# Kernel tuning notes

Measured on AMD Instinct MI355X. Metric: run time of the kernel, lower is better.

The kernel has to match this reference:

```python
import jax, jax.numpy as jnp
import numpy as np


def _gru(x, h0, Wi, Wh, bi, bh):
    """PyTorch-equations GRU. x: (T,B,D), Wi: (3H,D), Wh: (3H,H). Returns (ys, hT)."""
    xW = jnp.einsum('tbd,gd->tbg', x, Wi) + bi  # (T,B,3H) precomputed input proj
    def step(h, xw):
        hw = h @ Wh.T + bh
        xr, xz, xn = jnp.split(xw, 3, axis=-1)
        hr, hz, hn = jnp.split(hw, 3, axis=-1)
        r = jax.nn.sigmoid(xr + hr)
        z = jax.nn.sigmoid(xz + hz)
        n = jnp.tanh(xn + r * hn)
        h_new = (1.0 - z) * n + z * h
        return h_new, h_new
    hT, ys = jax.lax.scan(step, h0, xW)
    return ys, hT


def _bigru(x, WiF, WhF, biF, bhF, WiB, WhB, biB, bhB):
    B = x.shape[1]
    H = WhF.shape[1]
    h0 = jnp.zeros((B, H), x.dtype)
    yf, hf = _gru(x, h0, WiF, WhF, biF, bhF)
    yb, hb = _gru(x[::-1], h0, WiB, WhB, biB, bhB)
    return jnp.concatenate([yf, yb[::-1]], axis=-1), jnp.stack([hf, hb], axis=0)


def _ln(x, g, b, eps=1e-5):
    mu = x.mean(-1, keepdims=True)
    var = ((x - mu) ** 2).mean(-1, keepdims=True)
    return (x - mu) * jax.lax.rsqrt(var + eps) * g + b


def _forward(tokens, emb,
             s_WiF, s_WhF, s_biF, s_bhF, s_lnF_g, s_lnF_b,
             s_Wi_f, s_Wh_f, s_bi_f, s_bh_f, s_Wi_b, s_Wh_b, s_bi_b, s_bh_b,
             s_ln_g, s_ln_b, s_linW, s_linb,
             d_WiF, d_WhF, d_biF, d_bhF, d_lnF_g, d_lnF_b,
             d_Wi_f, d_Wh_f, d_bi_f, d_bh_f, d_Wi_b, d_Wh_b, d_bi_b, d_bh_b,
             d_ln_g, d_ln_b, out_W, out_b):
    S, T, B = tokens.shape
    H = s_WhF.shape[1]
    # sentence loop is batch-independent -> fold sentences into batch
    x = emb[tokens]                                  # (S,T,B,E)
    x = x.transpose(1, 0, 2, 3).reshape(T, S * B, -1)  # (T, S*B, E)
    h0 = jnp.zeros((S * B, H), x.dtype)
    y, _ = _gru(x, h0, s_WiF, s_WhF, s_biF, s_bhF)
    y = _ln(y, s_lnF_g, s_lnF_b)
    y, _ = _bigru(y, s_Wi_f, s_Wh_f, s_bi_f, s_bh_f, s_Wi_b, s_Wh_b, s_bi_b, s_bh_b)
    y = _ln(y, s_ln_g, s_ln_b)
    y = jnp.tanh(y @ s_linW.T + s_linb)              # (T, S*B, H)
    store = y.mean(axis=0).reshape(S, B, H)          # per-sentence mean-pooled cell
    # document-level encoder over sentence sequence
    h0d = jnp.zeros((B, H), x.dtype)
    y, _ = _gru(store, h0d, d_WiF, d_WhF, d_biF, d_bhF)
    y = _ln(y, d_lnF_g, d_lnF_b)
    y, _ = _bigru(y, d_Wi_f, d_Wh_f, d_bi_f, d_bh_f, d_Wi_b, d_Wh_b, d_bi_b, d_bh_b)
    y = _ln(y, d_ln_g, d_ln_b)
    return jax.nn.sigmoid(y @ out_W.T + out_b)       # (S, B, O)


def setup_inputs() -> dict:
    V, E, H, O = 32000, 256, 256, 2
    S, T, B = 96, 32, 32
    keys = iter(jax.random.split(jax.random.key(0), 64))
    def g(shape, scale=0.06):
        return jax.random.normal(next(keys), shape, jnp.float32) * scale
    inp = {}
    inp['tokens'] = jax.random.randint(next(keys), (S, T, B), 0, V)
    inp['emb'] = g((V, E), 0.1)
    # sentence encoder: uni GRU (E->H), LN(H), bi GRU (H->H), LN(2H), linear 2H->H
    inp['s_WiF'] = g((3 * H, E)); inp['s_WhF'] = g((3 * H, H))
    inp['s_biF'] = jnp.zeros((3 * H,)); inp['s_bhF'] = jnp.zeros((3 * H,))
    inp['s_lnF_g'] = jnp.ones((H,)); inp['s_lnF_b'] = jnp.zeros((H,))
    inp['s_Wi_f'] = g((3 * H, H)); inp['s_Wh_f'] = g((3 * H, H))
    inp['s_bi_f'] = jnp.zeros((3 * H,)); inp['s_bh_f'] = jnp.zeros((3 * H,))
    inp['s_Wi_b'] = g((3 * H, H)); inp['s_Wh_b'] = g((3 * H, H))
    inp['s_bi_b'] = jnp.zeros((3 * H,)); inp['s_bh_b'] = jnp.zeros((3 * H,))
    inp['s_ln_g'] = jnp.ones((2 * H,)); inp['s_ln_b'] = jnp.zeros((2 * H,))
    inp['s_linW'] = g((H, 2 * H)); inp['s_linb'] = jnp.zeros((H,))
    # document encoder: uni GRU (H->H), LN(H), bi GRU (H->H), LN(2H)
    inp['d_WiF'] = g((3 * H, H)); inp['d_WhF'] = g((3 * H, H))
    inp['d_biF'] = jnp.zeros((3 * H,)); inp['d_bhF'] = jnp.zeros((3 * H,))
    inp['d_lnF_g'] = jnp.ones((H,)); inp['d_lnF_b'] = jnp.zeros((H,))
    inp['d_Wi_f'] = g((3 * H, H)); inp['d_Wh_f'] = g((3 * H, H))
    inp['d_bi_f'] = jnp.zeros((3 * H,)); inp['d_bh_f'] = jnp.zeros((3 * H,))
    inp['d_Wi_b'] = g((3 * H, H)); inp['d_Wh_b'] = g((3 * H, H))
    inp['d_bi_b'] = jnp.zeros((3 * H,)); inp['d_bh_b'] = jnp.zeros((3 * H,))
    inp['d_ln_g'] = jnp.ones((2 * H,)); inp['d_ln_b'] = jnp.zeros((2 * H,))
    inp['out_W'] = g((O, 2 * H)); inp['out_b'] = jnp.zeros((O,))
    return inp


def reference(tokens, emb,
              s_WiF, s_WhF, s_biF, s_bhF, s_lnF_g, s_lnF_b,
              s_Wi_f, s_Wh_f, s_bi_f, s_bh_f, s_Wi_b, s_Wh_b, s_bi_b, s_bh_b,
              s_ln_g, s_ln_b, s_linW, s_linb,
              d_WiF, d_WhF, d_biF, d_bhF, d_lnF_g, d_lnF_b,
              d_Wi_f, d_Wh_f, d_bi_f, d_bh_f, d_Wi_b, d_Wh_b, d_bi_b, d_bh_b,
              d_ln_g, d_ln_b, out_W, out_b):
    return _forward(tokens, emb,
                    s_WiF, s_WhF, s_biF, s_bhF, s_lnF_g, s_lnF_b,
                    s_Wi_f, s_Wh_f, s_bi_f, s_bh_f, s_Wi_b, s_Wh_b, s_bi_b, s_bh_b,
                    s_ln_g, s_ln_b, s_linW, s_linb,
                    d_WiF, d_WhF, d_biF, d_bhF, d_lnF_g, d_lnF_b,
                    d_Wi_f, d_Wh_f, d_bi_f, d_bh_f, d_Wi_b, d_Wh_b, d_bi_b, d_bh_b,
                    d_ln_g, d_ln_b, out_W, out_b)
```

## Files before the change

### kernel.cpp

```cpp
#include <hip/hip_runtime.h>


typedef __bf16 bf16;
typedef __bf16 bf16x8 __attribute__((ext_vector_type(8)));
typedef __bf16 bf16x4 __attribute__((ext_vector_type(4)));
typedef float  f32x4  __attribute__((ext_vector_type(4)));

static __device__ __forceinline__ f32x4 mfma16(bf16x8 a, bf16x8 b, f32x4 c) {
  return __builtin_amdgcn_mfma_f32_16x16x32_bf16(a, b, c, 0, 0, 0);
}
static __device__ __forceinline__ float sigm(float x) { return 1.f / (1.f + __expf(-x)); }

__global__ __launch_bounds__(256) void cvt_bf16(
    const float* __restrict__ s, bf16* __restrict__ d, int n4)
{
  int i = blockIdx.x * 256 + threadIdx.x;
  if (i < n4) {
    float4 v = ((const float4*)s)[i];
    bf16x4 o;
    o[0] = (bf16)v.x; o[1] = (bf16)v.y; o[2] = (bf16)v.z; o[3] = (bf16)v.w;
    ((bf16x4*)d)[i] = o;
  }
}

__global__ __launch_bounds__(256) void conv13(
    const float* s0, const float* s1, const float* s2, const float* s3,
    const float* s4, const float* s5, const float* s6, const float* s7,
    const float* s8, const float* s9, const float* s10, const float* s11,
    const float* s12, bf16* __restrict__ dst)
{
  const float* srcs[13] = {s0,s1,s2,s3,s4,s5,s6,s7,s8,s9,s10,s11,s12};
  int m = blockIdx.y;
  int n4 = (m == 12) ? 32768 : 49152;
  int i = blockIdx.x * 256 + threadIdx.x;
  if (i >= n4) return;
  float4 v = ((const float4*)srcs[m])[i];
  bf16x4 o;
  o[0] = (bf16)v.x; o[1] = (bf16)v.y; o[2] = (bf16)v.z; o[3] = (bf16)v.w;
  ((bf16x4*)(dst + (size_t)m * 196608))[i] = o;
}

__global__ __launch_bounds__(256, 2) void gru_step(
    const bf16* __restrict__ xF, const bf16* __restrict__ hpF, bf16* __restrict__ hoF,
    const bf16* __restrict__ WiF, const bf16* __restrict__ WhF,
    const float* __restrict__ biF, const float* __restrict__ bhF,
    const bf16* __restrict__ xB, const bf16* __restrict__ hpB, bf16* __restrict__ hoB,
    const bf16* __restrict__ WiB, const bf16* __restrict__ WhB,
    const float* __restrict__ biB, const float* __restrict__ bhB,
    const int* __restrict__ tok, const bf16* __restrict__ embb, int t, int hstride)
{
  const bf16 *x, *hp, *Wi, *Wh;
  const float *bi, *bh;
  bf16* ho;
  if (blockIdx.y == 0) { x = xF; hp = hpF; ho = hoF; Wi = WiF; Wh = WhF; bi = biF; bh = bhF; }
  else                 { x = xB; hp = hpB; ho = hoB; Wi = WiB; Wh = WhB; bi = biB; bh = bhB; }

  int wv   = (threadIdx.x >> 6) + (blockIdx.x << 2);
  int cj   = (wv & 15) << 4;
  int m0   = (wv >> 4) << 5;
  int lane = threadIdx.x & 63;
  int r16  = lane & 15, g4 = lane >> 4;

  const bf16 *xp0, *xp1;
  if (x) {
    xp0 = x + (size_t)(m0 + r16) * 256;
    xp1 = xp0 + (size_t)16 * 256;
  } else {
    int n0 = m0 + r16, n1 = n0 + 16;
    int tk0 = tok[((n0 >> 5) << 10) + (t << 5) + (n0 & 31)];
    int tk1 = tok[((n1 >> 5) << 10) + (t << 5) + (n1 & 31)];
    xp0 = embb + (size_t)tk0 * 256;
    xp1 = embb + (size_t)tk1 * 256;
  }
  const bf16* wi = Wi + (size_t)(cj + r16) * 256;
  const bf16* wh = Wh + (size_t)(cj + r16) * 256;

  f32x4 Ar0 = {0,0,0,0}, Ar1 = {0,0,0,0};
  f32x4 Az0 = {0,0,0,0}, Az1 = {0,0,0,0};
  f32x4 Xn0 = {0,0,0,0}, Xn1 = {0,0,0,0};
  f32x4 Hn0 = {0,0,0,0}, Hn1 = {0,0,0,0};

#pragma unroll
  for (int kk = 0; kk < 8; kk++) {
    int k0 = kk * 32 + g4 * 8;
    bf16x8 a0 = *(const bf16x8*)(xp0 + k0);
    bf16x8 a1 = *(const bf16x8*)(xp1 + k0);
    bf16x8 wr = *(const bf16x8*)(wi + k0);
    bf16x8 wz = *(const bf16x8*)(wi + 65536 + k0);
    bf16x8 wn = *(const bf16x8*)(wi + 131072 + k0);
    Ar0 = mfma16(a0, wr, Ar0); Ar1 = mfma16(a1, wr, Ar1);
    Az0 = mfma16(a0, wz, Az0); Az1 = mfma16(a1, wz, Az1);
    Xn0 = mfma16(a0, wn, Xn0); Xn1 = mfma16(a1, wn, Xn1);
  }
  if (hp) {
    const bf16* hq0 = hp + (size_t)(m0 + r16) * hstride;
    const bf16* hq1 = hq0 + (size_t)16 * hstride;
#pragma unroll
    for (int kk = 0; kk < 8; kk++) {
      int k0 = kk * 32 + g4 * 8;
      bf16x8 a0 = *(const bf16x8*)(hq0 + k0);
      bf16x8 a1 = *(const bf16x8*)(hq1 + k0);
      bf16x8 wr = *(const bf16x8*)(wh + k0);
      bf16x8 wz = *(const bf16x8*)(wh + 65536 + k0);
      bf16x8 wn = *(const bf16x8*)(wh + 131072 + k0);
      Ar0 = mfma16(a0, wr, Ar0); Ar1 = mfma16(a1, wr, Ar1);
      Az0 = mfma16(a0, wz, Az0); Az1 = mfma16(a1, wz, Az1);
      Hn0 = mfma16(a0, wn, Hn0); Hn1 = mfma16(a1, wn, Hn1);
    }
  }

  float br = bi[cj + r16] + bh[cj + r16];
  float bz = bi[256 + cj + r16] + bh[256 + cj + r16];
  float bin = bi[512 + cj + r16], bhn = bh[512 + cj + r16];

#pragma unroll
  for (int rt = 0; rt < 2; rt++) {
    f32x4 Ar = rt ? Ar1 : Ar0, Az = rt ? Az1 : Az0;
    f32x4 Xn = rt ? Xn1 : Xn0, Hn = rt ? Hn1 : Hn0;
#pragma unroll
    for (int j = 0; j < 4; j++) {
      int orow = m0 + rt * 16 + g4 * 4 + j;
      float r = sigm(Ar[j] + br);
      float z = sigm(Az[j] + bz);
      float n = tanhf(Xn[j] + bin + r * (Hn[j] + bhn));
      float hpv = hp ? (float)hp[(size_t)orow * hstride + cj + r16] : 0.f;
      ho[(size_t)orow * hstride + cj + r16] = (bf16)((1.f - z) * n + z * hpv);
    }
  }
}

__global__ __launch_bounds__(256) void ln_rows(
    bf16* __restrict__ data, const float* __restrict__ gam, const float* __restrict__ bet,
    int rows, int D)
{
  int wid = threadIdx.x >> 6, lane = threadIdx.x & 63;
  int row = (blockIdx.x << 2) + wid;
  if (row >= rows) return;
  bf16* p = data + (size_t)row * D;
  int c = D >> 6;
  float v[8];
  float s = 0.f;
  if (c == 8) {
    bf16x8 t8 = *(const bf16x8*)(p + lane * 8);
#pragma unroll
    for (int j = 0; j < 8; j++) { v[j] = (float)t8[j]; s += v[j]; }
  } else {
    bf16x4 t4 = *(const bf16x4*)(p + lane * 4);
#pragma unroll
    for (int j = 0; j < 4; j++) { v[j] = (float)t4[j]; s += v[j]; }
#pragma unroll
    for (int j = 4; j < 8; j++) v[j] = 0.f;
  }
  float sq = 0.f;
  for (int j = 0; j < c; j++) sq += v[j] * v[j];
  for (int m = 32; m; m >>= 1) { s += __shfl_xor(s, m); sq += __shfl_xor(sq, m); }
  float invD = 1.f / (float)D;
  float mu  = s * invD;
  float var = sq * invD - mu * mu;
  float inv = rsqrtf(fmaxf(var, 0.f) + 1e-5f);
  int base = lane * c;
  for (int j = 0; j < c; j++) {
    float o = (v[j] - mu) * inv * gam[base + j] + bet[base + j];
    p[base + j] = (bf16)o;
  }
}

__global__ __launch_bounds__(256) void sent_tail(
    const bf16* __restrict__ hf, const bf16* __restrict__ hb,
    const float* __restrict__ gam, const float* __restrict__ bet,
    const bf16* __restrict__ W, const float* __restrict__ bias,
    bf16* __restrict__ store, int c, int row_base)
{
  int wave = threadIdx.x >> 6;
  int lane = threadIdx.x & 63;
  int r16 = lane & 15, g4 = lane >> 4;
  int r0 = (int)blockIdx.x << 4;
  size_t rowoff = (size_t)(r0 + r16) * 256;

  f32x4 ms0 = {0,0,0,0}, ms1 = {0,0,0,0}, ms2 = {0,0,0,0}, ms3 = {0,0,0,0};

  for (int t = 0; t < 32; t++) {
    const bf16* pf = hf + (size_t)t * c * 256 + rowoff;
    const bf16* pb = hb + (size_t)t * c * 256 + rowoff;
    bf16x8 xv[16];
    float s = 0.f, sq = 0.f;
#pragma unroll
    for (int kk = 0; kk < 16; kk++) {
      int k0 = kk * 32 + g4 * 8;
      xv[kk] = (kk < 8) ? *(const bf16x8*)(pf + k0) : *(const bf16x8*)(pb + k0 - 256);
#pragma unroll
      for (int j = 0; j < 8; j++) { float f = (float)xv[kk][j]; s += f; sq += f * f; }
    }
    s  += __shfl_xor(s, 16);  s  += __shfl_xor(s, 32);
    sq += __shfl_xor(sq, 16); sq += __shfl_xor(sq, 32);
    float mu  = s * (1.f / 512.f);
    float var = sq * (1.f / 512.f) - mu * mu;
    float inv = rsqrtf(fmaxf(var, 0.f) + 1e-5f);
#pragma unroll
    for (int kk = 0; kk < 16; kk++) {
      int k0 = kk * 32 + g4 * 8;
      float ga[8], be[8];
      *(float4*)(ga)     = *(const float4*)(gam + k0);
      *(float4*)(ga + 4) = *(const float4*)(gam + k0 + 4);
      *(float4*)(be)     = *(const float4*)(bet + k0);
      *(float4*)(be + 4) = *(const float4*)(bet + k0 + 4);
#pragma unroll
      for (int j = 0; j < 8; j++)
        xv[kk][j] = (bf16)(((float)xv[kk][j] - mu) * inv * ga[j] + be[j]);
    }
#pragma unroll
    for (int tc = 0; tc < 4; tc++) {
      int cj = wave * 64 + tc * 16;
      const bf16* wp = W + (size_t)(cj + r16) * 512;
      f32x4 acc = {0,0,0,0};
#pragma unroll
      for (int kk = 0; kk < 16; kk++)
        acc = mfma16(xv[kk], *(const bf16x8*)(wp + kk * 32 + g4 * 8), acc);
      float bb = bias[cj + r16];
      f32x4* msp = (tc == 0) ? &ms0 : (tc == 1) ? &ms1 : (tc == 2) ? &ms2 : &ms3;
#pragma unroll
      for (int j = 0; j < 4; j++) (*msp)[j] += tanhf(acc[j] + bb);
    }
  }
#pragma unroll
  for (int tc = 0; tc < 4; tc++) {
    int cj = wave * 64 + tc * 16;
    f32x4 ms = (tc == 0) ? ms0 : (tc == 1) ? ms1 : (tc == 2) ? ms2 : ms3;
#pragma unroll
    for (int j = 0; j < 4; j++) {
      int row = row_base + r0 + g4 * 4 + j;
      store[(size_t)row * 256 + cj + r16] = (bf16)(ms[j] * 0.03125f);
    }
  }
}

__global__ __launch_bounds__(256) void xw_gemm(
    const bf16* __restrict__ X,
    const bf16* __restrict__ W0, const float* __restrict__ b0, bf16* __restrict__ o0,
    const bf16* __restrict__ W1, const float* __restrict__ b1, bf16* __restrict__ o1)
{
  const bf16* W = blockIdx.y ? W1 : W0;
  const float* bias = blockIdx.y ? b1 : b0;
  bf16* out = blockIdx.y ? o1 : o0;
  int wave = (int)blockIdx.x * 4 + (threadIdx.x >> 6);
  int rt = wave / 48, ct = wave - rt * 48;
  int lane = threadIdx.x & 63;
  int r16 = lane & 15, g4 = lane >> 4;
  const bf16* ap = X + (size_t)(rt * 16 + r16) * 256;
  const bf16* wp = W + (size_t)(ct * 16 + r16) * 256;
  f32x4 acc = {0,0,0,0};
#pragma unroll
  for (int kk = 0; kk < 8; kk++) {
    int k0 = kk * 32 + g4 * 8;
    acc = mfma16(*(const bf16x8*)(ap + k0), *(const bf16x8*)(wp + k0), acc);
  }
  float bv = bias[ct * 16 + r16];
#pragma unroll
  for (int j = 0; j < 4; j++)
    out[(size_t)(rt * 16 + g4 * 4 + j) * 768 + ct * 16 + r16] = (bf16)(acc[j] + bv);
}

__global__ __launch_bounds__(1024, 4) void doc_gru(
    const bf16* __restrict__ xwF, const bf16* __restrict__ WhF_, const float* __restrict__ bhF_,
    const bf16* __restrict__ xwB, const bf16* __restrict__ WhB_, const float* __restrict__ bhB_,
    bf16* __restrict__ yout, int ostride,
    const float* __restrict__ lng, const float* __restrict__ lnb, int S)
{
  int dir = blockIdx.x;
  const bf16*  xw = dir ? xwB : xwF;
  const bf16*  Wh = dir ? WhB_ : WhF_;
  const float* bh = dir ? bhB_ : bhF_;
  int obase = dir ? 256 : 0;

  __shared__ bf16 hbuf[32][264];
  for (int idx = threadIdx.x; idx < 32 * 264; idx += 1024) ((bf16*)hbuf)[idx] = (bf16)0.f;
  __syncthreads();

  int w = threadIdx.x >> 6, lane = threadIdx.x & 63;
  int r16 = lane & 15, g4 = lane >> 4;
  int c = w * 16 + r16;
  const bf16* whp = Wh + (size_t)c * 256;
  float bhr = bh[c], bhz = bh[c + 256], bhn = bh[c + 512];

  for (int i = 0; i < S; i++) {
    int st = dir ? (S - 1 - i) : i;
    const bf16* xp = xw + (size_t)st * 24576;
    float xr[2][3][4];
#pragma unroll
    for (int rt = 0; rt < 2; rt++)
#pragma unroll
      for (int j = 0; j < 4; j++) {
        const bf16* q = xp + (size_t)(rt * 16 + g4 * 4 + j) * 768 + c;
        xr[rt][0][j] = (float)q[0];
        xr[rt][1][j] = (float)q[256];
        xr[rt][2][j] = (float)q[512];
      }
    float hp0[4], hp1[4];
#pragma unroll
    for (int j = 0; j < 4; j++) {
      hp0[j] = (float)hbuf[g4 * 4 + j][c];
      hp1[j] = (float)hbuf[16 + g4 * 4 + j][c];
    }
    f32x4 A00 = {0,0,0,0}, A01 = {0,0,0,0}, A02 = {0,0,0,0};
    f32x4 A10 = {0,0,0,0}, A11 = {0,0,0,0}, A12 = {0,0,0,0};
#pragma unroll
    for (int kk = 0; kk < 8; kk++) {
      int k0 = kk * 32 + g4 * 8;
      bf16x8 a0 = *(const bf16x8*)&hbuf[r16][k0];
      bf16x8 a1 = *(const bf16x8*)&hbuf[16 + r16][k0];
      bf16x8 w0 = *(const bf16x8*)(whp + k0);
      bf16x8 w1 = *(const bf16x8*)(whp + 65536 + k0);
      bf16x8 w2 = *(const bf16x8*)(whp + 131072 + k0);
      A00 = mfma16(a0, w0, A00); A10 = mfma16(a1, w0, A10);
      A01 = mfma16(a0, w1, A01); A11 = mfma16(a1, w1, A11);
      A02 = mfma16(a0, w2, A02); A12 = mfma16(a1, w2, A12);
    }
    float hnew[2][4];
#pragma unroll
    for (int rt = 0; rt < 2; rt++) {
      f32x4 A0 = rt ? A10 : A00, A1 = rt ? A11 : A01, A2 = rt ? A12 : A02;
#pragma unroll
      for (int j = 0; j < 4; j++) {
        float r = sigm(xr[rt][0][j] + A0[j] + bhr);
        float z = sigm(xr[rt][1][j] + A1[j] + bhz);
        float n = tanhf(xr[rt][2][j] + r * (A2[j] + bhn));
        float hpv = rt ? hp1[j] : hp0[j];
        hnew[rt][j] = (1.f - z) * n + z * hpv;
      }
    }
    __syncthreads();
#pragma unroll
    for (int rt = 0; rt < 2; rt++)
#pragma unroll
      for (int j = 0; j < 4; j++)
        hbuf[rt * 16 + g4 * 4 + j][c] = (bf16)hnew[rt][j];
    __syncthreads();
    if (lng) {
#pragma unroll
      for (int rr = 0; rr < 2; rr++) {
        int row = w * 2 + rr;
        bf16x4 v4 = *(const bf16x4*)&hbuf[row][lane * 4];
        float v[4]; float sm = 0.f, sq = 0.f;
#pragma unroll
        for (int j = 0; j < 4; j++) { v[j] = (float)v4[j]; sm += v[j]; sq += v[j] * v[j]; }
        for (int msk = 32; msk; msk >>= 1) { sm += __shfl_xor(sm, msk); sq += __shfl_xor(sq, msk); }
        float mu  = sm * (1.f / 256.f);
        float var = sq * (1.f / 256.f) - mu * mu;
        float inv = rsqrtf(fmaxf(var, 0.f) + 1e-5f);
        bf16x4 o;
#pragma unroll
        for (int j = 0; j < 4; j++)
          o[j] = (bf16)((v[j] - mu) * inv * lng[lane * 4 + j] + lnb[lane * 4 + j]);
        *(bf16x4*)&yout[((size_t)st * 32 + row) * ostride + lane * 4] = o;
      }
    } else {
#pragma unroll
      for (int rt = 0; rt < 2; rt++)
#pragma unroll
        for (int j = 0; j < 4; j++)
          yout[((size_t)st * 32 + rt * 16 + g4 * 4 + j) * ostride + obase + c] = (bf16)hnew[rt][j];
    }
  }
}

__global__ __launch_bounds__(256) void ln_out_head(
    const bf16* __restrict__ X, const float* __restrict__ lng, const float* __restrict__ lnb,
    const float* __restrict__ W, const float* __restrict__ bias, float* __restrict__ out)
{
  int w = threadIdx.x >> 6, lane = threadIdx.x & 63;
  int row = (int)blockIdx.x * 4 + w;
  bf16x8 v8 = *(const bf16x8*)&X[(size_t)row * 512 + lane * 8];
  float v[8]; float sm = 0.f, sq = 0.f;
#pragma unroll
  for (int j = 0; j < 8; j++) { v[j] = (float)v8[j]; sm += v[j]; sq += v[j] * v[j]; }
  for (int msk = 32; msk; msk >>= 1) { sm += __shfl_xor(sm, msk); sq += __shfl_xor(sq, msk); }
  float mu  = sm * (1.f / 512.f);
  float var = sq * (1.f / 512.f) - mu * mu;
  float inv = rsqrtf(fmaxf(var, 0.f) + 1e-5f);
  float a0 = 0.f, a1 = 0.f;
  int base = lane * 8;
#pragma unroll
  for (int j = 0; j < 8; j++) {
    float y = (v[j] - mu) * inv * lng[base + j] + lnb[base + j];
    a0 += y * W[base + j];
    a1 += y * W[512 + base + j];
  }
  for (int msk = 32; msk; msk >>= 1) { a0 += __shfl_xor(a0, msk); a1 += __shfl_xor(a1, msk); }
  if (lane == 0) {
    out[(size_t)row * 2 + 0] = sigm(a0 + bias[0]);
    out[(size_t)row * 2 + 1] = sigm(a1 + bias[1]);
  }
}

extern "C" void kernel_launch(void* const* d_in, const int* in_sizes, int n_in,
                              void* d_out, int out_size, void* d_ws, size_t ws_size,
                              hipStream_t stream)
{
  (void)in_sizes; (void)n_in; (void)out_size;
  const int*   tokens = (const int*)d_in[0];
  const float* emb    = (const float*)d_in[1];
  auto fp = [&](int i) { return (const float*)d_in[i]; };
  const float *s_WiF = fp(2),  *s_WhF = fp(3),  *s_biF = fp(4),  *s_bhF = fp(5);
  const float *s_lnF_g = fp(6), *s_lnF_b = fp(7);
  const float *s_Wi_f = fp(8),  *s_Wh_f = fp(9),  *s_bi_f = fp(10), *s_bh_f = fp(11);
  const float *s_Wi_b = fp(12), *s_Wh_b = fp(13), *s_bi_b = fp(14), *s_bh_b = fp(15);
  const float *s_ln_g = fp(16), *s_ln_b = fp(17), *s_linW = fp(18), *s_linb = fp(19);
  const float *dWiF = fp(20), *dWhF = fp(21), *dbiF = fp(22), *dbhF = fp(23);
  const float *d_lnF_g = fp(24), *d_lnF_b = fp(25);
  const float *dWi_f = fp(26), *dWh_f = fp(27), *dbi_f = fp(28), *dbh_f = fp(29);
  const float *dWi_b = fp(30), *dWh_b = fp(31), *dbi_b = fp(32), *dbh_b = fp(33);
  const float *d_ln_g = fp(34), *d_ln_b = fp(35), *out_W = fp(36), *out_b = fp(37);

  const int T = 32, S = 96;
  const int GW = 196608;

  bf16* wc = (bf16*)d_ws;
  bf16 *c_sWiF = wc,         *c_sWhF = wc + GW;
  bf16 *c_sWif = wc + 2*GW,  *c_sWhf = wc + 3*GW;
  bf16 *c_sWib = wc + 4*GW,  *c_sWhb = wc + 5*GW;
  bf16 *c_dWiF = wc + 6*GW,  *c_dWhF = wc + 7*GW;
  bf16 *c_dWif = wc + 8*GW,  *c_dWhf = wc + 9*GW;
  bf16 *c_dWib = wc + 10*GW, *c_dWhb = wc + 11*GW;
  bf16 *c_linW = wc + 12*GW;
  const size_t WB = (size_t)(12 * GW + 131072) * 2;
  bf16* embb = (bf16*)((char*)d_ws + WB);
  const size_t EB = (size_t)32000 * 256 * 2;

  conv13<<<dim3(192, 13), 256, 0, stream>>>(
      s_WiF, s_WhF, s_Wi_f, s_Wh_f, s_Wi_b, s_Wh_b,
      dWiF, dWhF, dWi_f, dWh_f, dWi_b, dWh_b, s_linW, wc);
  cvt_bf16<<<8000, 256, 0, stream>>>(emb, embb, 2048000);

  char* ws = (char*)d_ws + WB + EB;
  bf16* xw_u = (bf16*)ws;
  bf16* xw_f = xw_u + (size_t)3072 * 768;
  bf16* xw_b = xw_f + (size_t)3072 * 768;
  bf16* store = xw_b + (size_t)3072 * 768;
  bf16* yd1ln = store + (size_t)3072 * 256;
  bf16* ybid  = yd1ln + (size_t)3072 * 256;
  const size_t fixedB = WB + EB + ((size_t)3 * 3072 * 768
                      + (size_t)3072 * 256 * 2 + (size_t)3072 * 512) * 2;

  int c = 3072;
  while (c > 96 && fixedB + (size_t)3 * T * c * 512 > ws_size) c >>= 1;
  bf16* y1 = (bf16*)((char*)d_ws + fixedB);
  bf16* hf = y1 + (size_t)T * c * 256;
  bf16* hb = hf + (size_t)T * c * 256;
  const size_t cH = (size_t)c * 256;

  for (int base = 0; base < 3072; base += c) {
    const int* tkb = tokens + (size_t)base * 32;
    for (int t = 0; t < T; t++) {
      gru_step<<<dim3(c / 8, 1), 256, 0, stream>>>(
          nullptr, t ? y1 + (size_t)(t - 1) * cH : nullptr, y1 + (size_t)t * cH,
          c_sWiF, c_sWhF, s_biF, s_bhF,
          nullptr, nullptr, nullptr, nullptr, nullptr, nullptr, nullptr,
          tkb, embb, t, 256);
    }
    ln_rows<<<(T * c) / 4, 256, 0, stream>>>(y1, s_lnF_g, s_lnF_b, T * c, 256);
    for (int i = 0; i < T; i++) {
      int tb = T - 1 - i;
      gru_step<<<dim3(c / 8, 2), 256, 0, stream>>>(
          y1 + (size_t)i * cH,  i ? hf + (size_t)(i - 1) * cH : nullptr,  hf + (size_t)i * cH,
          c_sWif, c_sWhf, s_bi_f, s_bh_f,
          y1 + (size_t)tb * cH, i ? hb + (size_t)(tb + 1) * cH : nullptr, hb + (size_t)tb * cH,
          c_sWib, c_sWhb, s_bi_b, s_bh_b,
          nullptr, nullptr, 0, 256);
    }
    sent_tail<<<c / 16, 256, 0, stream>>>(hf, hb, s_ln_g, s_ln_b, c_linW, s_linb,
                                          store, c, base);
  }

  xw_gemm<<<dim3(2304, 1), 256, 0, stream>>>(store, c_dWiF, dbiF, xw_u,
                                             nullptr, nullptr, nullptr);
  doc_gru<<<dim3(1), 1024, 0, stream>>>(xw_u, c_dWhF, dbhF,
                                        nullptr, nullptr, nullptr,
                                        yd1ln, 256, d_lnF_g, d_lnF_b, S);
  xw_gemm<<<dim3(2304, 2), 256, 0, stream>>>(yd1ln, c_dWif, dbi_f, xw_f,
                                             c_dWib, dbi_b, xw_b);
  doc_gru<<<dim3(2), 1024, 0, stream>>>(xw_f, c_dWhf, dbh_f,
                                        xw_b, c_dWhb, dbh_b,
                                        ybid, 512, nullptr, nullptr, S);
  ln_out_head<<<768, 256, 0, stream>>>(ybid, d_ln_g, d_ln_b, out_W, out_b,
                                       (float*)d_out);
}
```

Measured before the change: 4.462 ms.

## Replace per-timestep GRU launches with persistent recurrent kernels and hoisted input GEMMs

```diff
diff --git a/kernel.cpp b/kernel.cpp
--- a/kernel.cpp
+++ b/kernel.cpp
@@ -38,200 +38,6 @@
   bf16x4 o;
   o[0] = (bf16)v.x; o[1] = (bf16)v.y; o[2] = (bf16)v.z; o[3] = (bf16)v.w;
   ((bf16x4*)(dst + (size_t)m * 196608))[i] = o;
-}
-
-__global__ __launch_bounds__(256, 2) void gru_step(
-    const bf16* __restrict__ xF, const bf16* __restrict__ hpF, bf16* __restrict__ hoF,
-    const bf16* __restrict__ WiF, const bf16* __restrict__ WhF,
-    const float* __restrict__ biF, const float* __restrict__ bhF,
-    const bf16* __restrict__ xB, const bf16* __restrict__ hpB, bf16* __restrict__ hoB,
-    const bf16* __restrict__ WiB, const bf16* __restrict__ WhB,
-    const float* __restrict__ biB, const float* __restrict__ bhB,
-    const int* __restrict__ tok, const bf16* __restrict__ embb, int t, int hstride)
-{
-  const bf16 *x, *hp, *Wi, *Wh;
-  const float *bi, *bh;
-  bf16* ho;
-  if (blockIdx.y == 0) { x = xF; hp = hpF; ho = hoF; Wi = WiF; Wh = WhF; bi = biF; bh = bhF; }
-  else                 { x = xB; hp = hpB; ho = hoB; Wi = WiB; Wh = WhB; bi = biB; bh = bhB; }
-
-  int wv   = (threadIdx.x >> 6) + (blockIdx.x << 2);
-  int cj   = (wv & 15) << 4;
-  int m0   = (wv >> 4) << 5;
-  int lane = threadIdx.x & 63;
-  int r16  = lane & 15, g4 = lane >> 4;
-
-  const bf16 *xp0, *xp1;
-  if (x) {
-    xp0 = x + (size_t)(m0 + r16) * 256;
-    xp1 = xp0 + (size_t)16 * 256;
-  } else {
-    int n0 = m0 + r16, n1 = n0 + 16;
-    int tk0 = tok[((n0 >> 5) << 10) + (t << 5) + (n0 & 31)];
-    int tk1 = tok[((n1 >> 5) << 10) + (t << 5) + (n1 & 31)];
-    xp0 = embb + (size_t)tk0 * 256;
-    xp1 = embb + (size_t)tk1 * 256;
-  }
-  const bf16* wi = Wi + (size_t)(cj + r16) * 256;
-  const bf16* wh = Wh + (size_t)(cj + r16) * 256;
-
-  f32x4 Ar0 = {0,0,0,0}, Ar1 = {0,0,0,0};
-  f32x4 Az0 = {0,0,0,0}, Az1 = {0,0,0,0};
-  f32x4 Xn0 = {0,0,0,0}, Xn1 = {0,0,0,0};
-  f32x4 Hn0 = {0,0,0,0}, Hn1 = {0,0,0,0};
-
-#pragma unroll
-  for (int kk = 0; kk < 8; kk++) {
-    int k0 = kk * 32 + g4 * 8;
-    bf16x8 a0 = *(const bf16x8*)(xp0 + k0);
-    bf16x8 a1 = *(const bf16x8*)(xp1 + k0);
-    bf16x8 wr = *(const bf16x8*)(wi + k0);
-    bf16x8 wz = *(const bf16x8*)(wi + 65536 + k0);
-    bf16x8 wn = *(const bf16x8*)(wi + 131072 + k0);
-    Ar0 = mfma16(a0, wr, Ar0); Ar1 = mfma16(a1, wr, Ar1);
-    Az0 = mfma16(a0, wz, Az0); Az1 = mfma16(a1, wz, Az1);
-    Xn0 = mfma16(a0, wn, Xn0); Xn1 = mfma16(a1, wn, Xn1);
-  }
-  if (hp) {
-    const bf16* hq0 = hp + (size_t)(m0 + r16) * hstride;
-    const bf16* hq1 = hq0 + (size_t)16 * hstride;
-#pragma unroll
-    for (int kk = 0; kk < 8; kk++) {
-      int k0 = kk * 32 + g4 * 8;
-      bf16x8 a0 = *(const bf16x8*)(hq0 + k0);
-      bf16x8 a1 = *(const bf16x8*)(hq1 + k0);
-      bf16x8 wr = *(const bf16x8*)(wh + k0);
-      bf16x8 wz = *(const bf16x8*)(wh + 65536 + k0);
-      bf16x8 wn = *(const bf16x8*)(wh + 131072 + k0);
-      Ar0 = mfma16(a0, wr, Ar0); Ar1 = mfma16(a1, wr, Ar1);
-      Az0 = mfma16(a0, wz, Az0); Az1 = mfma16(a1, wz, Az1);
-      Hn0 = mfma16(a0, wn, Hn0); Hn1 = mfma16(a1, wn, Hn1);
-    }
-  }
-
-  float br = bi[cj + r16] + bh[cj + r16];
-  float bz = bi[256 + cj + r16] + bh[256 + cj + r16];
-  float bin = bi[512 + cj + r16], bhn = bh[512 + cj + r16];
-
-#pragma unroll
-  for (int rt = 0; rt < 2; rt++) {
-    f32x4 Ar = rt ? Ar1 : Ar0, Az = rt ? Az1 : Az0;
-    f32x4 Xn = rt ? Xn1 : Xn0, Hn = rt ? Hn1 : Hn0;
-#pragma unroll
-    for (int j = 0; j < 4; j++) {
-      int orow = m0 + rt * 16 + g4 * 4 + j;
-      float r = sigm(Ar[j] + br);
-      float z = sigm(Az[j] + bz);
-      float n = tanhf(Xn[j] + bin + r * (Hn[j] + bhn));
-      float hpv = hp ? (float)hp[(size_t)orow * hstride + cj + r16] : 0.f;
-      ho[(size_t)orow * hstride + cj + r16] = (bf16)((1.f - z) * n + z * hpv);
-    }
-  }
-}
-
-__global__ __launch_bounds__(256) void ln_rows(
-    bf16* __restrict__ data, const float* __restrict__ gam, const float* __restrict__ bet,
-    int rows, int D)
-{
-  int wid = threadIdx.x >> 6, lane = threadIdx.x & 63;
-  int row = (blockIdx.x << 2) + wid;
-  if (row >= rows) return;
-  bf16* p = data + (size_t)row * D;
-  int c = D >> 6;
-  float v[8];
-  float s = 0.f;
-  if (c == 8) {
-    bf16x8 t8 = *(const bf16x8*)(p + lane * 8);
-#pragma unroll
-    for (int j = 0; j < 8; j++) { v[j] = (float)t8[j]; s += v[j]; }
-  } else {
-    bf16x4 t4 = *(const bf16x4*)(p + lane * 4);
-#pragma unroll
-    for (int j = 0; j < 4; j++) { v[j] = (float)t4[j]; s += v[j]; }
-#pragma unroll
-    for (int j = 4; j < 8; j++) v[j] = 0.f;
-  }
-  float sq = 0.f;
-  for (int j = 0; j < c; j++) sq += v[j] * v[j];
-  for (int m = 32; m; m >>= 1) { s += __shfl_xor(s, m); sq += __shfl_xor(sq, m); }
-  float invD = 1.f / (float)D;
-  float mu  = s * invD;
-  float var = sq * invD - mu * mu;
-  float inv = rsqrtf(fmaxf(var, 0.f) + 1e-5f);
-  int base = lane * c;
-  for (int j = 0; j < c; j++) {
-    float o = (v[j] - mu) * inv * gam[base + j] + bet[base + j];
-    p[base + j] = (bf16)o;
-  }
-}
-
-__global__ __launch_bounds__(256) void sent_tail(
-    const bf16* __restrict__ hf, const bf16* __restrict__ hb,
-    const float* __restrict__ gam, const float* __restrict__ bet,
-    const bf16* __restrict__ W, const float* __restrict__ bias,
-    bf16* __restrict__ store, int c, int row_base)
-{
-  int wave = threadIdx.x >> 6;
-  int lane = threadIdx.x & 63;
-  int r16 = lane & 15, g4 = lane >> 4;
-  int r0 = (int)blockIdx.x << 4;
-  size_t rowoff = (size_t)(r0 + r16) * 256;
-
-  f32x4 ms0 = {0,0,0,0}, ms1 = {0,0,0,0}, ms2 = {0,0,0,0}, ms3 = {0,0,0,0};
-
-  for (int t = 0; t < 32; t++) {
-    const bf16* pf = hf + (size_t)t * c * 256 + rowoff;
-    const bf16* pb = hb + (size_t)t * c * 256 + rowoff;
-    bf16x8 xv[16];
-    float s = 0.f, sq = 0.f;
-#pragma unroll
-    for (int kk = 0; kk < 16; kk++) {
-      int k0 = kk * 32 + g4 * 8;
-      xv[kk] = (kk < 8) ? *(const bf16x8*)(pf + k0) : *(const bf16x8*)(pb + k0 - 256);
-#pragma unroll
-      for (int j = 0; j < 8; j++) { float f = (float)xv[kk][j]; s += f; sq += f * f; }
-    }
-    s  += __shfl_xor(s, 16);  s  += __shfl_xor(s, 32);
-    sq += __shfl_xor(sq, 16); sq += __shfl_xor(sq, 32);
-    float mu  = s * (1.f / 512.f);
-    float var = sq * (1.f / 512.f) - mu * mu;
-    float inv = rsqrtf(fmaxf(var, 0.f) + 1e-5f);
-#pragma unroll
-    for (int kk = 0; kk < 16; kk++) {
-      int k0 = kk * 32 + g4 * 8;
-      float ga[8], be[8];
-      *(float4*)(ga)     = *(const float4*)(gam + k0);
-      *(float4*)(ga + 4) = *(const float4*)(gam + k0 + 4);
-      *(float4*)(be)     = *(const float4*)(bet + k0);
-      *(float4*)(be + 4) = *(const float4*)(bet + k0 + 4);
-#pragma unroll
-      for (int j = 0; j < 8; j++)
-        xv[kk][j] = (bf16)(((float)xv[kk][j] - mu) * inv * ga[j] + be[j]);
-    }
-#pragma unroll
-    for (int tc = 0; tc < 4; tc++) {
-      int cj = wave * 64 + tc * 16;
-      const bf16* wp = W + (size_t)(cj + r16) * 512;
-      f32x4 acc = {0,0,0,0};
-#pragma unroll
-      for (int kk = 0; kk < 16; kk++)
-        acc = mfma16(xv[kk], *(const bf16x8*)(wp + kk * 32 + g4 * 8), acc);
-      float bb = bias[cj + r16];
-      f32x4* msp = (tc == 0) ? &ms0 : (tc == 1) ? &ms1 : (tc == 2) ? &ms2 : &ms3;
-#pragma unroll
-      for (int j = 0; j < 4; j++) (*msp)[j] += tanhf(acc[j] + bb);
-    }
-  }
-#pragma unroll
-  for (int tc = 0; tc < 4; tc++) {
-    int cj = wave * 64 + tc * 16;
-    f32x4 ms = (tc == 0) ? ms0 : (tc == 1) ? ms1 : (tc == 2) ? ms2 : ms3;
-#pragma unroll
-    for (int j = 0; j < 4; j++) {
-      int row = row_base + r0 + g4 * 4 + j;
-      store[(size_t)row * 256 + cj + r16] = (bf16)(ms[j] * 0.03125f);
-    }
-  }
 }
 
 __global__ __launch_bounds__(256) void xw_gemm(
@@ -260,86 +66,162 @@
     out[(size_t)(rt * 16 + g4 * 4 + j) * 768 + ct * 16 + r16] = (bf16)(acc[j] + bv);
 }
 
-__global__ __launch_bounds__(1024, 4) void doc_gru(
-    const bf16* __restrict__ xwF, const bf16* __restrict__ WhF_, const float* __restrict__ bhF_,
-    const bf16* __restrict__ xwB, const bf16* __restrict__ WhB_, const float* __restrict__ bhB_,
-    bf16* __restrict__ yout, int ostride,
-    const float* __restrict__ lng, const float* __restrict__ lnb, int S)
-{
-  int dir = blockIdx.x;
+__global__ __launch_bounds__(256) void xw_gather_gemm(
+    const int* __restrict__ tok, const bf16* __restrict__ embb,
+    const bf16* __restrict__ W, const float* __restrict__ bias,
+    bf16* __restrict__ out, int c)
+{
+  int t = blockIdx.y;
+  int wave = (int)blockIdx.x * 4 + (threadIdx.x >> 6);
+  int rt = wave / 48, ct = wave - rt * 48;
+  int lane = threadIdx.x & 63;
+  int r16 = lane & 15, g4 = lane >> 4;
+  int n = rt * 16 + r16;
+  int tk = tok[((n >> 5) << 10) + (t << 5) + (n & 31)];
+  const bf16* ap = embb + (size_t)tk * 256;
+  const bf16* wp = W + (size_t)(ct * 16 + r16) * 256;
+  f32x4 acc = {0,0,0,0};
+#pragma unroll
+  for (int kk = 0; kk < 8; kk++) {
+    int k0 = kk * 32 + g4 * 8;
+    acc = mfma16(*(const bf16x8*)(ap + k0), *(const bf16x8*)(wp + k0), acc);
+  }
+  float bv = bias[ct * 16 + r16];
+#pragma unroll
+  for (int j = 0; j < 4; j++)
+    out[((size_t)t * c + rt * 16 + g4 * 4 + j) * 768 + ct * 16 + r16] = (bf16)(acc[j] + bv);
+}
+
+__global__ __launch_bounds__(512, 2) void pgru(
+    const bf16* __restrict__ xwF, const bf16* __restrict__ WhF, const float* __restrict__ bhF,
+    const bf16* __restrict__ xwB, const bf16* __restrict__ WhB, const float* __restrict__ bhB,
+    bf16* __restrict__ youtF, bf16* __restrict__ youtB, int ostride,
+    const float* __restrict__ lng, const float* __restrict__ lnb,
+    int steps, int Mtot)
+{
+  int dir = blockIdx.y;
   const bf16*  xw = dir ? xwB : xwF;
-  const bf16*  Wh = dir ? WhB_ : WhF_;
-  const float* bh = dir ? bhB_ : bhF_;
-  int obase = dir ? 256 : 0;
-
-  __shared__ bf16 hbuf[32][264];
-  for (int idx = threadIdx.x; idx < 32 * 264; idx += 1024) ((bf16*)hbuf)[idx] = (bf16)0.f;
-  __syncthreads();
-
-  int w = threadIdx.x >> 6, lane = threadIdx.x & 63;
-  int r16 = lane & 15, g4 = lane >> 4;
-  int c = w * 16 + r16;
-  const bf16* whp = Wh + (size_t)c * 256;
-  float bhr = bh[c], bhz = bh[c + 256], bhn = bh[c + 512];
-
-  for (int i = 0; i < S; i++) {
-    int st = dir ? (S - 1 - i) : i;
-    const bf16* xp = xw + (size_t)st * 24576;
-    float xr[2][3][4];
-#pragma unroll
-    for (int rt = 0; rt < 2; rt++)
-#pragma unroll
-      for (int j = 0; j < 4; j++) {
-        const bf16* q = xp + (size_t)(rt * 16 + g4 * 4 + j) * 768 + c;
-        xr[rt][0][j] = (float)q[0];
-        xr[rt][1][j] = (float)q[256];
-        xr[rt][2][j] = (float)q[512];
-      }
-    float hp0[4], hp1[4];
-#pragma unroll
-    for (int j = 0; j < 4; j++) {
-      hp0[j] = (float)hbuf[g4 * 4 + j][c];
-      hp1[j] = (float)hbuf[16 + g4 * 4 + j][c];
-    }
-    f32x4 A00 = {0,0,0,0}, A01 = {0,0,0,0}, A02 = {0,0,0,0};
-    f32x4 A10 = {0,0,0,0}, A11 = {0,0,0,0}, A12 = {0,0,0,0};
+  const bf16*  Wh = dir ? WhB : WhF;
+  const float* bh = dir ? bhB : bhF;
+  bf16* yout = dir ? youtB : youtF;
+
+  __shared__ bf16 hbuf[16][264];
+  __shared__ bf16 xbuf[2][16][776];
+
+  int tid = threadIdx.x;
+  int w = tid >> 6, lane = tid & 63, r16 = lane & 15, g4 = lane >> 4;
+  int rowbase = (int)blockIdx.x * 16;
+  int cb = w * 32;
+  int c0 = cb + r16, c1 = cb + 16 + r16;
+
+  for (int i2 = tid; i2 < 528; i2 += 512) ((bf16x8*)hbuf)[i2] = (bf16x8){};
+
+  bf16x8 wr0[8], wz0[8], wn0[8], wr1[8], wz1[8], wn1[8];
+  {
+    const bf16* W0 = Wh + (size_t)c0 * 256;
+    const bf16* W1 = Wh + (size_t)c1 * 256;
 #pragma unroll
     for (int kk = 0; kk < 8; kk++) {
       int k0 = kk * 32 + g4 * 8;
-      bf16x8 a0 = *(const bf16x8*)&hbuf[r16][k0];
-      bf16x8 a1 = *(const bf16x8*)&hbuf[16 + r16][k0];
-      bf16x8 w0 = *(const bf16x8*)(whp + k0);
-      bf16x8 w1 = *(const bf16x8*)(whp + 65536 + k0);
-      bf16x8 w2 = *(const bf16x8*)(whp + 131072 + k0);
-      A00 = mfma16(a0, w0, A00); A10 = mfma16(a1, w0, A10);
-      A01 = mfma16(a0, w1, A01); A11 = mfma16(a1, w1, A11);
-      A02 = mfma16(a0, w2, A02); A12 = mfma16(a1, w2, A12);
-    }
-    float hnew[2][4];
-#pragma unroll
-    for (int rt = 0; rt < 2; rt++) {
-      f32x4 A0 = rt ? A10 : A00, A1 = rt ? A11 : A01, A2 = rt ? A12 : A02;
+      wr0[kk] = *(const bf16x8*)(W0 + k0);
+      wz0[kk] = *(const bf16x8*)(W0 + 65536 + k0);
+      wn0[kk] = *(const bf16x8*)(W0 + 131072 + k0);
+      wr1[kk] = *(const bf16x8*)(W1 + k0);
+      wz1[kk] = *(const bf16x8*)(W1 + 65536 + k0);
+      wn1[kk] = *(const bf16x8*)(W1 + 131072 + k0);
+    }
+  }
+  float bhr0 = bh[c0], bhz0 = bh[c0 + 256], bhn0 = bh[c0 + 512];
+  float bhr1 = bh[c1], bhz1 = bh[c1 + 256], bhn1 = bh[c1 + 512];
+
+  {
+    int st0 = dir ? steps - 1 : 0;
+    const bf16* src = xw + ((size_t)st0 * Mtot + rowbase) * 768;
+#pragma unroll
+    for (int it = 0; it < 3; it++) {
+      int idx = it * 4096 + tid * 8;
+      bf16x8 v = *(const bf16x8*)(src + idx);
+      int m = idx / 768, k = idx - m * 768;
+      *(bf16x8*)&xbuf[0][m][k] = v;
+    }
+  }
+  __syncthreads();
+
+  for (int i = 0; i < steps; i++) {
+    int cur = i & 1;
+    int st = dir ? steps - 1 - i : i;
+    bf16x8 pf0 = {}, pf1 = {}, pf2 = {};
+    bool havepf = (i + 1 < steps);
+    if (havepf) {
+      int stn = dir ? steps - 2 - i : i + 1;
+      const bf16* src = xw + ((size_t)stn * Mtot + rowbase) * 768;
+      pf0 = *(const bf16x8*)(src + tid * 8);
+      pf1 = *(const bf16x8*)(src + 4096 + tid * 8);
+      pf2 = *(const bf16x8*)(src + 8192 + tid * 8);
+    }
+    f32x4 ar0 = {0,0,0,0}, az0 = {0,0,0,0}, an0 = {0,0,0,0};
+    f32x4 ar1 = {0,0,0,0}, az1 = {0,0,0,0}, an1 = {0,0,0,0};
+#pragma unroll
+    for (int kk = 0; kk < 8; kk++) {
+      bf16x8 a = *(const bf16x8*)&hbuf[r16][kk * 32 + g4 * 8];
+      ar0 = mfma16(a, wr0[kk], ar0); az0 = mfma16(a, wz0[kk], az0); an0 = mfma16(a, wn0[kk], an0);
+      ar1 = mfma16(a, wr1[kk], ar1); az1 = mfma16(a, wz1[kk], az1); an1 = mfma16(a, wn1[kk], an1);
+    }
+    float hn0[4], hn1[4];
+#pragma unroll
+    for (int j = 0; j < 4; j++) {
+      int m = g4 * 4 + j;
+      const bf16* xq = &xbuf[cur][m][0];
+      {
+        float r = sigm((float)xq[c0] + ar0[j] + bhr0);
+        float z = sigm((float)xq[c0 + 256] + az0[j] + bhz0);
+        float n = tanhf((float)xq[c0 + 512] + r * (an0[j] + bhn0));
+        float hp = (float)hbuf[m][c0];
+        hn0[j] = (1.f - z) * n + z * hp;
+      }
+      {
+        float r = sigm((float)xq[c1] + ar1[j] + bhr1);
+        float z = sigm((float)xq[c1 + 256] + az1[j] + bhz1);
+        float n = tanhf((float)xq[c1 + 512] + r * (an1[j] + bhn1));
+        float hp = (float)hbuf[m][c1];
+        hn1[j] = (1.f - z) * n + z * hp;
+      }
+    }
+    __syncthreads();
+#pragma unroll
+    for (int j = 0; j < 4; j++) {
+      int m = g4 * 4 + j;
+      hbuf[m][c0] = (bf16)hn0[j];
+      hbuf[m][c1] = (bf16)hn1[j];
+    }
+    if (havepf) {
+      {
+        int idx = tid * 8;            int m = idx / 768, k = idx - m * 768;
+        *(bf16x8*)&xbuf[cur ^ 1][m][k] = pf0;
+      }
+      {
+        int idx = 4096 + tid * 8;     int m = idx / 768, k = idx - m * 768;
+        *(bf16x8*)&xbuf[cur ^ 1][m][k] = pf1;
+      }
+      {
+        int idx = 8192 + tid * 8;     int m = idx / 768, k = idx - m * 768;
+        *(bf16x8*)&xbuf[cur ^ 1][m][k] = pf2;
+      }
+    }
+    if (!lng) {
 #pragma unroll
       for (int j = 0; j < 4; j++) {
-        float r = sigm(xr[rt][0][j] + A0[j] + bhr);
-        float z = sigm(xr[rt][1][j] + A1[j] + bhz);
-        float n = tanhf(xr[rt][2][j] + r * (A2[j] + bhn));
-        float hpv = rt ? hp1[j] : hp0[j];
-        hnew[rt][j] = (1.f - z) * n + z * hpv;
-      }
-    }
-    __syncthreads();
-#pragma unroll
-    for (int rt = 0; rt < 2; rt++)
-#pragma unroll
-      for (int j = 0; j < 4; j++)
-        hbuf[rt * 16 + g4 * 4 + j][c] = (bf16)hnew[rt][j];
+        size_t ro = ((size_t)st * Mtot + rowbase + g4 * 4 + j) * ostride;
+        yout[ro + c0] = (bf16)hn0[j];
+        yout[ro + c1] = (bf16)hn1[j];
+      }
+    }
     __syncthreads();
     if (lng) {
 #pragma unroll
       for (int rr = 0; rr < 2; rr++) {
-        int row = w * 2 + rr;
-        bf16x4 v4 = *(const bf16x4*)&hbuf[row][lane * 4];
+        int r = w * 2 + rr;
+        bf16x4 v4 = *(const bf16x4*)&hbuf[r][lane * 4];
         float v[4]; float sm = 0.f, sq = 0.f;
 #pragma unroll
         for (int j = 0; j < 4; j++) { v[j] = (float)v4[j]; sm += v[j]; sq += v[j] * v[j]; }
@@ -351,14 +233,77 @@
 #pragma unroll
         for (int j = 0; j < 4; j++)
           o[j] = (bf16)((v[j] - mu) * inv * lng[lane * 4 + j] + lnb[lane * 4 + j]);
-        *(bf16x4*)&yout[((size_t)st * 32 + row) * ostride + lane * 4] = o;
-      }
-    } else {
-#pragma unroll
-      for (int rt = 0; rt < 2; rt++)
-#pragma unroll
-        for (int j = 0; j < 4; j++)
-          yout[((size_t)st * 32 + rt * 16 + g4 * 4 + j) * ostride + obase + c] = (bf16)hnew[rt][j];
+        *(bf16x4*)&yout[((size_t)st * Mtot + rowbase + r) * ostride + lane * 4] = o;
+      }
+    }
+  }
+}
+
+__global__ __launch_bounds__(256) void sent_tail(
+    const bf16* __restrict__ hf, const bf16* __restrict__ hb,
+    const float* __restrict__ gam, const float* __restrict__ bet,
+    const bf16* __restrict__ W, const float* __restrict__ bias,
+    bf16* __restrict__ store, int c, int row_base)
+{
+  int wave = threadIdx.x >> 6;
+  int lane = threadIdx.x & 63;
+  int r16 = lane & 15, g4 = lane >> 4;
+  int r0 = (int)blockIdx.x << 4;
+  size_t rowoff = (size_t)(r0 + r16) * 256;
+
+  f32x4 ms0 = {0,0,0,0}, ms1 = {0,0,0,0}, ms2 = {0,0,0,0}, ms3 = {0,0,0,0};
+
+  for (int t = 0; t < 32; t++) {
+    const bf16* pf = hf + (size_t)t * c * 256 + rowoff;
+    const bf16* pb = hb + (size_t)t * c * 256 + rowoff;
+    bf16x8 xv[16];
+    float s = 0.f, sq = 0.f;
+#pragma unroll
+    for (int kk = 0; kk < 16; kk++) {
+      int k0 = kk * 32 + g4 * 8;
+      xv[kk] = (kk < 8) ? *(const bf16x8*)(pf + k0) : *(const bf16x8*)(pb + k0 - 256);
+#pragma unroll
+      for (int j = 0; j < 8; j++) { float f = (float)xv[kk][j]; s += f; sq += f * f; }
+    }
+    s  += __shfl_xor(s, 16);  s  += __shfl_xor(s, 32);
+    sq += __shfl_xor(sq, 16); sq += __shfl_xor(sq, 32);
+    float mu  = s * (1.f / 512.f);
+    float var = sq * (1.f / 512.f) - mu * mu;
+    float inv = rsqrtf(fmaxf(var, 0.f) + 1e-5f);
+#pragma unroll
+    for (int kk = 0; kk < 16; kk++) {
+      int k0 = kk * 32 + g4 * 8;
+      float ga[8], be[8];
+      *(float4*)(ga)     = *(const float4*)(gam + k0);
+      *(float4*)(ga + 4) = *(const float4*)(gam + k0 + 4);
+      *(float4*)(be)     = *(const float4*)(bet + k0);
+      *(float4*)(be + 4) = *(const float4*)(bet + k0 + 4);
+#pragma unroll
+      for (int j = 0; j < 8; j++)
+        xv[kk][j] = (bf16)(((float)xv[kk][j] - mu) * inv * ga[j] + be[j]);
+    }
+#pragma unroll
+    for (int tc = 0; tc < 4; tc++) {
+      int cj = wave * 64 + tc * 16;
+      const bf16* wp = W + (size_t)(cj + r16) * 512;
+      f32x4 acc = {0,0,0,0};
+#pragma unroll
+      for (int kk = 0; kk < 16; kk++)
+        acc = mfma16(xv[kk], *(const bf16x8*)(wp + kk * 32 + g4 * 8), acc);
+      float bb = bias[cj + r16];
+      f32x4* msp = (tc == 0) ? &ms0 : (tc == 1) ? &ms1 : (tc == 2) ? &ms2 : &ms3;
+#pragma unroll
+      for (int j = 0; j < 4; j++) (*msp)[j] += tanhf(acc[j] + bb);
+    }
+  }
+#pragma unroll
+  for (int tc = 0; tc < 4; tc++) {
+    int cj = wave * 64 + tc * 16;
+    f32x4 ms = (tc == 0) ? ms0 : (tc == 1) ? ms1 : (tc == 2) ? ms2 : ms3;
+#pragma unroll
+    for (int j = 0; j < 4; j++) {
+      int row = row_base + r0 + g4 * 4 + j;
+      store[(size_t)row * 256 + cj + r16] = (bf16)(ms[j] * 0.03125f);
     }
   }
 }
@@ -432,55 +377,51 @@
   cvt_bf16<<<8000, 256, 0, stream>>>(emb, embb, 2048000);
 
   char* ws = (char*)d_ws + WB + EB;
-  bf16* xw_u = (bf16*)ws;
-  bf16* xw_f = xw_u + (size_t)3072 * 768;
-  bf16* xw_b = xw_f + (size_t)3072 * 768;
-  bf16* store = xw_b + (size_t)3072 * 768;
+  bf16* store = (bf16*)ws;
   bf16* yd1ln = store + (size_t)3072 * 256;
   bf16* ybid  = yd1ln + (size_t)3072 * 256;
-  const size_t fixedB = WB + EB + ((size_t)3 * 3072 * 768
-                      + (size_t)3072 * 256 * 2 + (size_t)3072 * 512) * 2;
+  bf16* xw_u  = ybid  + (size_t)3072 * 512;
+  bf16* xwdf  = xw_u  + (size_t)3072 * 768;
+  bf16* xwdb  = xwdf  + (size_t)3072 * 768;
+  const size_t fixedB = WB + EB
+      + ((size_t)3072 * 256 * 2 + (size_t)3072 * 512 + (size_t)3 * 3072 * 768) * 2;
 
   int c = 3072;
-  while (c > 96 && fixedB + (size_t)3 * T * c * 512 > ws_size) c >>= 1;
-  bf16* y1 = (bf16*)((char*)d_ws + fixedB);
-  bf16* hf = y1 + (size_t)T * c * 256;
-  bf16* hb = hf + (size_t)T * c * 256;
-  const size_t cH = (size_t)c * 256;
+  while (c > 96 && fixedB + (size_t)196608 * c > ws_size) c >>= 1;
+  char* cb = (char*)d_ws + fixedB;
+  bf16* xw1  = (bf16*)cb;
+  bf16* y1ln = (bf16*)(cb + (size_t)49152 * c);
+  bf16* xwf  = (bf16*)(cb + (size_t)65536 * c);
+  bf16* xwb  = (bf16*)(cb + (size_t)114688 * c);
+  bf16* hf   = (bf16*)(cb + (size_t)163840 * c);
+  bf16* hb   = (bf16*)(cb + (size_t)180224 * c);
 
   for (int base = 0; base < 3072; base += c) {
     const int* tkb = tokens + (size_t)base * 32;
-    for (int t = 0; t < T; t++) {
-      gru_step<<<dim3(c / 8, 1), 256, 0, stream>>>(
-          nullptr, t ? y1 + (size_t)(t - 1) * cH : nullptr, y1 + (size_t)t * cH,
-          c_sWiF, c_sWhF, s_biF, s_bhF,
-          nullptr, nullptr, nullptr, nullptr, nullptr, nullptr, nullptr,
-          tkb, embb, t, 256);
-    }
-    ln_rows<<<(T * c) / 4, 256, 0, stream>>>(y1, s_lnF_g, s_lnF_b, T * c, 256);
-    for (int i = 0; i < T; i++) {
-      int tb = T - 1 - i;
-      gru_step<<<dim3(c / 8, 2), 256, 0, stream>>>(
-          y1 + (size_t)i * cH,  i ? hf + (size_t)(i - 1) * cH : nullptr,  hf + (size_t)i * cH,
-          c_sWif, c_sWhf, s_bi_f, s_bh_f,
-          y1 + (size_t)tb * cH, i ? hb + (size_t)(tb + 1) * cH : nullptr, hb + (size_t)tb * cH,
-          c_sWib, c_sWhb, s_bi_b, s_bh_b,
-          nullptr, nullptr, 0, 256);
-    }
+    xw_gather_gemm<<<dim3((c / 16) * 12, T), 256, 0, stream>>>(
+        tkb, embb, c_sWiF, s_biF, xw1, c);
+    pgru<<<dim3(c / 16, 1), 512, 0, stream>>>(
+        xw1, c_sWhF, s_bhF, nullptr, nullptr, nullptr,
+        y1ln, nullptr, 256, s_lnF_g, s_lnF_b, T, c);
+    xw_gemm<<<dim3(((T * c) / 16) * 12, 2), 256, 0, stream>>>(
+        y1ln, c_sWif, s_bi_f, xwf, c_sWib, s_bi_b, xwb);
+    pgru<<<dim3(c / 16, 2), 512, 0, stream>>>(
+        xwf, c_sWhf, s_bh_f, xwb, c_sWhb, s_bh_b,
+        hf, hb, 256, nullptr, nullptr, T, c);
     sent_tail<<<c / 16, 256, 0, stream>>>(hf, hb, s_ln_g, s_ln_b, c_linW, s_linb,
                                           store, c, base);
   }
 
-  xw_gemm<<<dim3(2304, 1), 256, 0, stream>>>(store, c_dWiF, dbiF, xw_u,
-                                             nullptr, nullptr, nullptr);
-  doc_gru<<<dim3(1), 1024, 0, stream>>>(xw_u, c_dWhF, dbhF,
-                                        nullptr, nullptr, nullptr,
-                                        yd1ln, 256, d_lnF_g, d_lnF_b, S);
-  xw_gemm<<<dim3(2304, 2), 256, 0, stream>>>(yd1ln, c_dWif, dbi_f, xw_f,
-                                             c_dWib, dbi_b, xw_b);
-  doc_gru<<<dim3(2), 1024, 0, stream>>>(xw_f, c_dWhf, dbh_f,
-                                        xw_b, c_dWhb, dbh_b,
-                                        ybid, 512, nullptr, nullptr, S);
+  xw_gemm<<<dim3((3072 / 16) * 12, 1), 256, 0, stream>>>(
+      store, c_dWiF, dbiF, xw_u, nullptr, nullptr, nullptr);
+  pgru<<<dim3(2, 1), 512, 0, stream>>>(
+      xw_u, c_dWhF, dbhF, nullptr, nullptr, nullptr,
+      yd1ln, nullptr, 256, d_lnF_g, d_lnF_b, S, 32);
+  xw_gemm<<<dim3((3072 / 16) * 12, 2), 256, 0, stream>>>(
+      yd1ln, c_dWif, dbi_f, xwdf, c_dWib, dbi_b, xwdb);
+  pgru<<<dim3(2, 2), 512, 0, stream>>>(
+      xwdf, c_dWhf, dbh_f, xwdb, c_dWhb, dbh_b,
+      ybid, ybid + 256, 512, nullptr, nullptr, S, 32);
   ln_out_head<<<768, 256, 0, stream>>>(ybid, d_ln_g, d_ln_b, out_W, out_b,
                                        (float*)d_out);
 }
```

Result: slower. 5.804 ms (+30.1%).
